# Kernel tuning notes

Hardware: AMD Instinct MI355X
Metric: run time of the kernel (lower is better)

Reference implementation:

```python
import jax, jax.numpy as jnp
import numpy as np

NUM_HEADS = 4
LN_EPS = 1e-5
L2_EPS = 1e-12


def setup_inputs() -> dict:
    key = jax.random.key(0)
    ks = jax.random.split(key, 10)
    B, L, D, Hd = 256, 197, 768, 512
    dh = Hd // NUM_HEADS  # 128
    NC = 1000
    sc = lambda k, shape, s: jax.random.normal(k, shape, jnp.float32) * s
    return {
        "cls_token": jax.random.normal(ks[0], (B, D), jnp.float32),
        "x": jax.random.normal(ks[1], (B, L, D), jnp.float32),
        "proj_w": sc(ks[2], (D, Hd), 0.02),
        "proj_b": jnp.zeros((Hd,), jnp.float32),
        "ln_g": jnp.ones((dh,), jnp.float32),
        "ln_b": jnp.zeros((dh,), jnp.float32),
        "conv1_w": sc(ks[3], (3, 3, 3, 3), 0.2),
        "conv2_w": sc(ks[4], (3, 3, 3, 3), 0.2),
        "cls1_w": sc(ks[5], (D, NC), 0.02),
        "cls1_b": jnp.zeros((NC,), jnp.float32),
        "cls2_w": sc(ks[6], (2883, NC), 0.02),
        "cls2_b": jnp.zeros((NC,), jnp.float32),
    }


def reference(cls_token, x, proj_w, proj_b, ln_g, ln_b, conv1_w, conv2_w,
              cls1_w, cls1_b, cls2_w, cls2_b):
    B, L, D = x.shape
    dh = ln_g.shape[0]
    # proj on patch tokens (drop cls at position 0)
    xp = x[:, 1:, :] @ proj_w + proj_b            # (B, 196, 512)
    Lp = xp.shape[1]
    H = xp.shape[2] // dh
    heads = xp.reshape(B, Lp, H, dh).transpose(2, 0, 1, 3)  # (H, B, Lp, dh)
    # LayerNorm over last dim (eps=1e-5, biased var, affine)
    mu = heads.mean(-1, keepdims=True)
    var = heads.var(-1, keepdims=True)
    hn = (heads - mu) * jax.lax.rsqrt(var + LN_EPS) * ln_g + ln_b
    # Covariance._remove_mean: adaptive_avg_pool2d on (B, dh, Lp) -> mean over BOTH dh and Lp per sample
    hn = hn - hn.mean(axis=(2, 3), keepdims=True)
    # 'near' cross-covariances between adjacent heads, all pairs batched
    x1, x2 = hn[:-1], hn[1:]                      # (H-1, B, Lp, dh)
    cov = jnp.einsum('pbnd,pbne->pbde', x1, x2) / Lp  # (H-1, B, dh, dh)
    # L2 normalize over dim=2 (row axis of each dh x dh map), F.normalize eps
    nrm = jnp.sqrt(jnp.sum(cov * cov, axis=2, keepdims=True))
    cov = cov / jnp.maximum(nrm, L2_EPS)
    cov = cov.transpose(1, 0, 2, 3)               # (B, 3, 128, 128)
    conv = lambda z, w: jax.lax.conv_general_dilated(
        z, w, (2, 2), 'VALID', dimension_numbers=('NCHW', 'OIHW', 'NCHW'))
    z = conv(cov, conv1_w)                        # (B, 3, 63, 63)
    z = jax.nn.gelu(z, approximate=False)
    z = conv(z, conv2_w)                          # (B, 3, 31, 31)
    flat = z.reshape(B, -1)                       # (B, 2883)
    out = ((cls_token @ cls1_w + cls1_b) + (flat @ cls2_w + cls2_b)) / 2
    return out
```

## Files before the change

### kernel.cpp

```cpp
#include <hip/hip_runtime.h>
#include <hip/hip_bf16.h>
#include <cstdint>

typedef __bf16 bf16_t;
typedef __bf16 bf16x4 __attribute__((ext_vector_type(4)));
typedef __bf16 bf16x8 __attribute__((ext_vector_type(8)));
typedef float floatx4 __attribute__((ext_vector_type(4)));

#define LNEPS 1e-5f

__device__ inline void async_copy16(const bf16_t* g, bf16_t* l) {
    __builtin_amdgcn_global_load_lds((const __attribute__((address_space(1))) void*)g,
                                     (__attribute__((address_space(3))) void*)l,
                                     16, 0, 0);
}

__global__ __launch_bounds__(256)
void k_cvt_x(const float* __restrict__ x, bf16_t* __restrict__ xbf) {
    const int vid = blockIdx.x * 256 + threadIdx.x;
    const int row = vid / 96;
    const int kv  = vid - row * 96;
    const int b = row / 196, l = row - (row / 196) * 196;
    const float* src = x + ((b * 197 + l + 1) * 96 + kv) * 8;
    const floatx4 f0 = *(const floatx4*)src;
    const floatx4 f1 = *(const floatx4*)(src + 4);
    bf16x8 o;
#pragma unroll
    for (int e = 0; e < 4; e++) { o[e] = (bf16_t)f0[e]; o[e+4] = (bf16_t)f1[e]; }
    *(bf16x8*)(xbf + vid * 8) = o;
}

__global__ __launch_bounds__(256)
void k_transpose_w(const float* __restrict__ w, bf16_t* __restrict__ wt) {
    __shared__ bf16_t tile[32][33];
    const int bx = blockIdx.x;
    const int by = blockIdx.y;
    const int tx = threadIdx.x & 31, ty = threadIdx.x >> 5;
    for (int i = ty; i < 32; i += 8)
        tile[i][tx] = (bf16_t)w[(by*32 + i)*512 + bx*32 + tx];
    __syncthreads();
    for (int i = ty; i < 32; i += 8)
        wt[(bx*32 + i)*768 + by*32 + tx] = tile[tx][i];
}

__global__ __launch_bounds__(256, 3)
void k_proj_ln(const bf16_t* __restrict__ xbf, const bf16_t* __restrict__ wt,
               const float* __restrict__ pb, const float* __restrict__ lng,
               const float* __restrict__ lnb, bf16_t* __restrict__ hn)
{
    __shared__ bf16_t As[2][128*32];
    __shared__ bf16_t Bs[2][128*32];

    const int t = threadIdx.x;
    const int lane = t & 63;
    const int wv = t >> 6;
    const int q = lane >> 4;
    const int c = lane & 15;
    const int h  = blockIdx.x;
    const int m0 = blockIdx.y * 128;

    const int srow  = t >> 2;
    const int skoff = (t & 3) * 8;
    const bf16_t* ag = xbf + (m0 + srow) * 768 + skoff;
    const bf16_t* bg = wt + (h*128 + srow) * 768 + skoff;

    floatx4 acc[2][8];
#pragma unroll
    for (int i = 0; i < 2; i++)
#pragma unroll
        for (int j = 0; j < 8; j++)
#pragma unroll
            for (int r = 0; r < 4; r++) acc[i][j][r] = 0.f;

    async_copy16(ag,           &As[0][t*8]);
    async_copy16(ag + 64*768,  &As[0][2048 + t*8]);
    async_copy16(bg,           &Bs[0][t*8]);
    async_copy16(bg + 64*768,  &Bs[0][2048 + t*8]);
    __syncthreads();

    int buf = 0;
    for (int ks = 0; ks < 24; ks++) {
        if (ks < 23) {
            const int kn = (ks + 1) * 32;
            async_copy16(ag + kn,           &As[buf^1][t*8]);
            async_copy16(ag + 64*768 + kn,  &As[buf^1][2048 + t*8]);
            async_copy16(bg + kn,           &Bs[buf^1][t*8]);
            async_copy16(bg + 64*768 + kn,  &Bs[buf^1][2048 + t*8]);
        }
        bf16x8 af[2], bfr[8];
#pragma unroll
        for (int i = 0; i < 2; i++)
            af[i] = *(const bf16x8*)&As[buf][(wv*32 + i*16 + c)*32 + q*8];
#pragma unroll
        for (int j = 0; j < 8; j++)
            bfr[j] = *(const bf16x8*)&Bs[buf][(j*16 + c)*32 + q*8];
#pragma unroll
        for (int i = 0; i < 2; i++)
#pragma unroll
            for (int j = 0; j < 8; j++)
                acc[i][j] = __builtin_amdgcn_mfma_f32_16x16x32_bf16(af[i], bfr[j], acc[i][j], 0, 0, 0);
        __syncthreads();
        buf ^= 1;
    }

    float bias[8], gg[8], bb[8];
#pragma unroll
    for (int j = 0; j < 8; j++) {
        const int d = j*16 + c;
        bias[j] = pb[h*128 + d];
        gg[j]   = lng[d];
        bb[j]   = lnb[d];
    }
#pragma unroll
    for (int i = 0; i < 2; i++) {
#pragma unroll
        for (int r = 0; r < 4; r++) {
            float s = 0.f, s2 = 0.f;
#pragma unroll
            for (int j = 0; j < 8; j++) {
                const float v = acc[i][j][r] + bias[j];
                acc[i][j][r] = v;
                s += v; s2 += v*v;
            }
#pragma unroll
            for (int o = 1; o < 16; o <<= 1) { s += __shfl_xor(s, o); s2 += __shfl_xor(s2, o); }
            const float mu = s * (1.f/128.f);
            const float ms = s2 * (1.f/128.f);
            const float rstd = rsqrtf(ms - mu*mu + LNEPS);
            const int gm = m0 + wv*32 + i*16 + q*4 + r;
            const int bI = gm / 196, l = gm - bI*196;
            bf16_t* dst = hn + (((h*256 + bI)*196 + l) << 7);
#pragma unroll
            for (int j = 0; j < 8; j++) {
                const float v = (acc[i][j][r] - mu)*rstd*gg[j] + bb[j];
                dst[j*16 + c] = (bf16_t)v;
            }
        }
    }
}

__global__ __launch_bounds__(256)
void k_colsum(const bf16_t* __restrict__ hn, float* __restrict__ colsum)
{
    __shared__ float tmp[16][128];
    const int t = threadIdx.x;
    const int g = t >> 4;
    const int dv = t & 15;
    const bf16_t* S = hn + ((long)blockIdx.x * 196 << 7) + dv * 8;
    float s[8] = {0.f,0.f,0.f,0.f,0.f,0.f,0.f,0.f};
    for (int n = g; n < 196; n += 16) {
        const bf16x8 v = *(const bf16x8*)(S + (n << 7));
#pragma unroll
        for (int e = 0; e < 8; e++) s[e] += (float)v[e];
    }
#pragma unroll
    for (int e = 0; e < 8; e++) tmp[g][dv*8 + e] = s[e];
    __syncthreads();
    if (t < 128) {
        float a = 0.f;
#pragma unroll
        for (int g2 = 0; g2 < 16; g2++) a += tmp[g2][t];
        colsum[(blockIdx.x << 7) + t] = a;
    }
}

__global__ __launch_bounds__(256, 2)
void k_cov(const bf16_t* __restrict__ hn, const float* __restrict__ colsum,
           float* __restrict__ cov)
{
    __shared__ bf16_t x1s[128*40];
    __shared__ bf16_t x2s[128*40];
    __shared__ float rs1[128], rs2[128];
    __shared__ float colsq[2][128];
    __shared__ float nrm_inv[128];
    __shared__ float mu_s[2];

    const int t = threadIdx.x;
    const int lane = t & 63;
    const int wv = t >> 6;
    const int wr = wv >> 1, wc = wv & 1;
    const int q = lane >> 4;
    const int c = lane & 15;
    const int b = blockIdx.x;
    const int p = blockIdx.y;

    const bf16_t* X1 = hn + (((p*256 + b)*196) << 7);
    const bf16_t* X2 = hn + ((((p+1)*256 + b)*196) << 7);

    if (t < 128) rs1[t] = colsum[((p*256 + b) << 7) + t];
    else         rs2[t & 127] = colsum[(((p+1)*256 + b) << 7) + (t & 127)];
    __syncthreads();
    if (wv == 0) {
        float s = rs1[lane] + rs1[lane + 64];
#pragma unroll
        for (int o = 1; o < 64; o <<= 1) s += __shfl_xor(s, o);
        if (lane == 0) mu_s[0] = s * (1.f/(196.f*128.f));
    } else if (wv == 1) {
        float s = rs2[lane] + rs2[lane + 64];
#pragma unroll
        for (int o = 1; o < 64; o <<= 1) s += __shfl_xor(s, o);
        if (lane == 0) mu_s[1] = s * (1.f/(196.f*128.f));
    }

    floatx4 acc[4][4];
#pragma unroll
    for (int i = 0; i < 4; i++)
#pragma unroll
        for (int j = 0; j < 4; j++)
#pragma unroll
            for (int r = 0; r < 4; r++) acc[i][j][r] = 0.f;

    const int nl = t >> 3;
    const int d0 = (t & 7) * 16;

    for (int n0 = 0; n0 < 224; n0 += 32) {
        __syncthreads();
        const int n = n0 + nl;
        bf16x8 va, vb, wa, wb;
        if (n < 196) {
            const bf16_t* s1 = X1 + (n << 7) + d0;
            const bf16_t* s2 = X2 + (n << 7) + d0;
            va = *(const bf16x8*)s1;
            vb = *(const bf16x8*)(s1 + 8);
            wa = *(const bf16x8*)s2;
            wb = *(const bf16x8*)(s2 + 8);
        } else {
#pragma unroll
            for (int e = 0; e < 8; e++) {
                va[e] = (bf16_t)0.f; vb[e] = (bf16_t)0.f;
                wa[e] = (bf16_t)0.f; wb[e] = (bf16_t)0.f;
            }
        }
#pragma unroll
        for (int e = 0; e < 8; e++) {
            x1s[(d0 + e)*40 + nl]     = va[e];
            x1s[(d0 + 8 + e)*40 + nl] = vb[e];
            x2s[(d0 + e)*40 + nl]     = wa[e];
            x2s[(d0 + 8 + e)*40 + nl] = wb[e];
        }
        __syncthreads();
        bf16x8 af[4], bfr[4];
#pragma unroll
        for (int i = 0; i < 4; i++)
            af[i] = *(const bf16x8*)&x1s[(wr*64 + i*16 + c)*40 + q*8];
#pragma unroll
        for (int j = 0; j < 4; j++)
            bfr[j] = *(const bf16x8*)&x2s[(wc*64 + j*16 + c)*40 + q*8];
#pragma unroll
        for (int i = 0; i < 4; i++)
#pragma unroll
            for (int j = 0; j < 4; j++)
                acc[i][j] = __builtin_amdgcn_mfma_f32_16x16x32_bf16(af[i], bfr[j], acc[i][j], 0, 0, 0);
    }

    const float mu1 = mu_s[0], mu2 = mu_s[1];
    const float invL = 1.f/196.f;
    float csq[4] = {0.f, 0.f, 0.f, 0.f};
#pragma unroll
    for (int i = 0; i < 4; i++)
#pragma unroll
        for (int j = 0; j < 4; j++)
#pragma unroll
            for (int r = 0; r < 4; r++) {
                const int d = wr*64 + i*16 + q*4 + r;
                const int e = wc*64 + j*16 + c;
                const float v = acc[i][j][r]*invL - mu2*rs1[d]*invL - mu1*rs2[e]*invL + mu1*mu2;
                acc[i][j][r] = v;
                csq[j] += v*v;
            }
#pragma unroll
    for (int j = 0; j < 4; j++) {
        float s = csq[j];
        s += __shfl_xor(s, 16);
        s += __shfl_xor(s, 32);
        csq[j] = s;
    }
    if (q == 0) {
#pragma unroll
        for (int j = 0; j < 4; j++) colsq[wr][wc*64 + j*16 + c] = csq[j];
    }
    __syncthreads();
    if (t < 128) {
        const float nr = sqrtf(colsq[0][t] + colsq[1][t]);
        nrm_inv[t] = 1.f / fmaxf(nr, 1e-12f);
    }
    __syncthreads();
    float* dst = cov + ((long)b*3 + p)*16384;
#pragma unroll
    for (int i = 0; i < 4; i++)
#pragma unroll
        for (int j = 0; j < 4; j++) {
            const int e = wc*64 + j*16 + c;
            const float ni = nrm_inv[e];
#pragma unroll
            for (int r = 0; r < 4; r++) {
                const int d = wr*64 + i*16 + q*4 + r;
                dst[(d << 7) + e] = acc[i][j][r] * ni;
            }
        }
}

__global__ __launch_bounds__(256)
void k_convs(const float* __restrict__ cov, const float* __restrict__ w1,
             const float* __restrict__ w2, bf16_t* __restrict__ Xb)
{
    __shared__ float Z[3*3969];
    __shared__ float W1s[81];
    __shared__ float W2s[81];
    const int t = threadIdx.x, b = blockIdx.x;
    if (t < 81) { W1s[t] = w1[t]; W2s[t] = w2[t]; }
    __syncthreads();
    const float* C = cov + (long)b*3*16384;
    for (int idx = t; idx < 3*3969; idx += 256) {
        const int o = idx / 3969, rem = idx - o*3969;
        const int y = rem / 63, xx = rem - y*63;
        float a = 0.f;
#pragma unroll
        for (int i = 0; i < 3; i++) {
            const float* Ci = C + i*16384 + (2*y)*128 + 2*xx;
            const float* Wi = &W1s[o*27 + i*9];
            a += Ci[0]*Wi[0]   + Ci[1]*Wi[1]   + Ci[2]*Wi[2]
               + Ci[128]*Wi[3] + Ci[129]*Wi[4] + Ci[130]*Wi[5]
               + Ci[256]*Wi[6] + Ci[257]*Wi[7] + Ci[258]*Wi[8];
        }
        Z[idx] = 0.5f*a*(1.0f + erff(a*0.70710678118654752f));
    }
    __syncthreads();
    for (int idx = t; idx < 2883; idx += 256) {
        const int o = idx / 961, rem = idx - o*961;
        const int y = rem / 31, xx = rem - y*31;
        float a = 0.f;
#pragma unroll
        for (int i = 0; i < 3; i++) {
            const float* Zi = Z + i*3969 + (2*y)*63 + 2*xx;
            const float* Wi = &W2s[(o*3+i)*9];
            a += Zi[0]*Wi[0]   + Zi[1]*Wi[1]   + Zi[2]*Wi[2]
               + Zi[63]*Wi[3]  + Zi[64]*Wi[4]  + Zi[65]*Wi[5]
               + Zi[126]*Wi[6] + Zi[127]*Wi[7] + Zi[128]*Wi[8];
        }
        Xb[(long)b*3712 + 768 + idx] = (bf16_t)a;
    }
}

__global__ __launch_bounds__(256)
void k_cvt_cls(const float* __restrict__ cls, bf16_t* __restrict__ Xb)
{
    const int t = threadIdx.x, b = blockIdx.x;
    for (int k = t; k < 768; k += 256)
        Xb[b*3712 + k] = (bf16_t)cls[b*768 + k];
    if (t < 61) Xb[b*3712 + 3651 + t] = (bf16_t)0.f;
}

__global__ __launch_bounds__(256)
void k_cvt_w(const float* __restrict__ W1, const float* __restrict__ W2,
             bf16_t* __restrict__ Wb)
{
    __shared__ bf16_t tile[32][33];
    const int k0 = blockIdx.x * 32;
    const int n0 = blockIdx.y * 32;
    const int tx = threadIdx.x & 31, ty = threadIdx.x >> 5;
    for (int i = ty; i < 32; i += 8) {
        const int k = k0 + i, n = n0 + tx;
        float v = 0.f;
        if (n < 1000 && k < 3651)
            v = (k < 768) ? W1[k*1000 + n] : W2[(k-768)*1000 + n];
        tile[i][tx] = (bf16_t)v;
    }
    __syncthreads();
    for (int i = ty; i < 32; i += 8)
        Wb[(n0 + i)*3712 + k0 + tx] = tile[tx][i];
}

__global__ __launch_bounds__(256, 2)
void k_gemm_cls(const bf16_t* __restrict__ Xb, const bf16_t* __restrict__ Wb,
                float* __restrict__ partial)
{
    __shared__ bf16_t As[128*32];
    __shared__ bf16_t Bs[128*32];

    const int t = threadIdx.x;
    const int lane = t & 63;
    const int wv = t >> 6;
    const int wr = wv >> 1, wc = wv & 1;
    const int q = lane >> 4;
    const int c = lane & 15;
    const int nt = blockIdx.x;
    const int mt = blockIdx.y;
    const int sp = blockIdx.z;

    const int srow  = t >> 2;
    const int skoff = (t & 3) * 8;
    const int m0 = mt * 128, n0 = nt * 128;
    const int kbase = sp * 928;
    const bf16_t* ag0 = Xb + (m0 + srow) * 3712 + kbase + skoff;
    const bf16_t* ag1 = Xb + (m0 + srow + 64) * 3712 + kbase + skoff;
    const bf16_t* bg0 = Wb + (n0 + srow) * 3712 + kbase + skoff;
    const bf16_t* bg1 = Wb + (n0 + srow + 64) * 3712 + kbase + skoff;

    floatx4 acc[4][4];
#pragma unroll
    for (int i = 0; i < 4; i++)
#pragma unroll
        for (int j = 0; j < 4; j++)
#pragma unroll
            for (int r = 0; r < 4; r++) acc[i][j][r] = 0.f;

    for (int k0 = 0; k0 < 928; k0 += 32) {
        __syncthreads();
        async_copy16(ag0 + k0, &As[t*8]);
        async_copy16(ag1 + k0, &As[2048 + t*8]);
        async_copy16(bg0 + k0, &Bs[t*8]);
        async_copy16(bg1 + k0, &Bs[2048 + t*8]);
        __syncthreads();
        bf16x8 af[4], bfr[4];
#pragma unroll
        for (int i = 0; i < 4; i++)
            af[i] = *(const bf16x8*)&As[(wr*64 + i*16 + c)*32 + q*8];
#pragma unroll
        for (int j = 0; j < 4; j++)
            bfr[j] = *(const bf16x8*)&Bs[(wc*64 + j*16 + c)*32 + q*8];
#pragma unroll
        for (int i = 0; i < 4; i++)
#pragma unroll
            for (int j = 0; j < 4; j++)
                acc[i][j] = __builtin_amdgcn_mfma_f32_16x16x32_bf16(af[i], bfr[j], acc[i][j], 0, 0, 0);
    }

    float* base = partial + ((long)sp*256 + m0)*1024 + n0;
#pragma unroll
    for (int i = 0; i < 4; i++)
#pragma unroll
        for (int r = 0; r < 4; r++) {
            const int row = wr*64 + i*16 + q*4 + r;
#pragma unroll
            for (int j = 0; j < 4; j++)
                base[row*1024 + wc*64 + j*16 + c] = acc[i][j][r];
        }
}

__global__ __launch_bounds__(256)
void k_cls_fin(const float* __restrict__ partial, const float* __restrict__ b1,
               const float* __restrict__ b2, float* __restrict__ out)
{
    const int idx = blockIdx.x * 256 + threadIdx.x;
    const int m = idx / 1000, n = idx - m*1000;
    float s = partial[(m)*1024 + n] + partial[(256 + m)*1024 + n]
            + partial[(512 + m)*1024 + n] + partial[(768 + m)*1024 + n];
    out[idx] = 0.5f*(s + b1[n] + b2[n]);
}

extern "C" void kernel_launch(void* const* d_in, const int* in_sizes, int n_in,
                              void* d_out, int out_size, void* d_ws, size_t ws_size,
                              hipStream_t stream) {
    const float* cls = (const float*)d_in[0];
    const float* x   = (const float*)d_in[1];
    const float* pw  = (const float*)d_in[2];
    const float* pb  = (const float*)d_in[3];
    const float* lng = (const float*)d_in[4];
    const float* lnb = (const float*)d_in[5];
    const float* c1w = (const float*)d_in[6];
    const float* c2w = (const float*)d_in[7];
    const float* w1  = (const float*)d_in[8];
    const float* b1  = (const float*)d_in[9];
    const float* w2  = (const float*)d_in[10];
    const float* b2  = (const float*)d_in[11];

    char* ws = (char*)d_ws;
    bf16_t* hn    = (bf16_t*)(ws);
    bf16_t* xbf   = (bf16_t*)(ws + 51380224ull);
    bf16_t* wt    = (bf16_t*)(ws + 128450560ull);
    float*  covb  = (float*) (ws + 51380224ull);
    float*  csum  = (float*) (ws + 129236992ull);
    bf16_t* Xb    = (bf16_t*)(ws + 129761280ull);
    bf16_t* Wb    = (bf16_t*)(ws + 131661824ull);
    float*  part  = (float*) (ws + 139264000ull);
    float*  out   = (float*)d_out;

    k_transpose_w<<<dim3(16, 24), 256, 0, stream>>>(pw, wt);
    k_cvt_x<<<18816, 256, 0, stream>>>(x, xbf);
    k_cvt_cls<<<256, 256, 0, stream>>>(cls, Xb);
    k_cvt_w<<<dim3(116, 32), 256, 0, stream>>>(w1, w2, Wb);
    k_proj_ln<<<dim3(4, 392), 256, 0, stream>>>(xbf, wt, pb, lng, lnb, hn);
    k_colsum<<<1024, 256, 0, stream>>>(hn, csum);
    k_cov<<<dim3(256, 3), 256, 0, stream>>>(hn, csum, covb);
    k_convs<<<256, 256, 0, stream>>>(covb, c1w, c2w, Xb);
    k_gemm_cls<<<dim3(8, 2, 4), 256, 0, stream>>>(Xb, Wb, part);
    k_cls_fin<<<1000, 256, 0, stream>>>(part, b1, b2, out);
}
```

Measured before the change: 439.4 us.

## Fuse fp32-to-bf16 conversion and column sums into projection kernel; split convs

The projection+LayerNorm kernel now reads fp32 activations directly, converts them to bf16 in registers and stores them to LDS, so the separate conversion pass and its bf16 intermediate buffer go away. The per-sample column sums are accumulated in the epilogue and added with atomics, which removes the separate colsum kernel (the sums are zeroed in the cls conversion kernel). The conv kernel is split into two row halves per sample to double the block count. The A loads are now synchronous register loads instead of async LDS copies, which may expose latency, and the fp32 atomics make the summation order nondeterministic.

```diff
diff --git a/kernel.cpp b/kernel.cpp
--- a/kernel.cpp
+++ b/kernel.cpp
@@ -13,21 +13,6 @@
     __builtin_amdgcn_global_load_lds((const __attribute__((address_space(1))) void*)g,
                                      (__attribute__((address_space(3))) void*)l,
                                      16, 0, 0);
-}
-
-__global__ __launch_bounds__(256)
-void k_cvt_x(const float* __restrict__ x, bf16_t* __restrict__ xbf) {
-    const int vid = blockIdx.x * 256 + threadIdx.x;
-    const int row = vid / 96;
-    const int kv  = vid - row * 96;
-    const int b = row / 196, l = row - (row / 196) * 196;
-    const float* src = x + ((b * 197 + l + 1) * 96 + kv) * 8;
-    const floatx4 f0 = *(const floatx4*)src;
-    const floatx4 f1 = *(const floatx4*)(src + 4);
-    bf16x8 o;
-#pragma unroll
-    for (int e = 0; e < 4; e++) { o[e] = (bf16_t)f0[e]; o[e+4] = (bf16_t)f1[e]; }
-    *(bf16x8*)(xbf + vid * 8) = o;
 }
 
 __global__ __launch_bounds__(256)
@@ -44,9 +29,10 @@
 }
 
 __global__ __launch_bounds__(256, 3)
-void k_proj_ln(const bf16_t* __restrict__ xbf, const bf16_t* __restrict__ wt,
+void k_proj_ln(const float* __restrict__ x, const bf16_t* __restrict__ wt,
                const float* __restrict__ pb, const float* __restrict__ lng,
-               const float* __restrict__ lnb, bf16_t* __restrict__ hn)
+               const float* __restrict__ lnb, bf16_t* __restrict__ hn,
+               float* __restrict__ csum)
 {
     __shared__ bf16_t As[2][128*32];
     __shared__ bf16_t Bs[2][128*32];
@@ -59,9 +45,15 @@
     const int h  = blockIdx.x;
     const int m0 = blockIdx.y * 128;
 
+    const int arow = t >> 1;
+    const int acol = (t & 1) * 16;
+    const int agm  = m0 + arow;
+    const int ab   = agm / 196;
+    const int al   = agm - ab * 196;
+    const float* ag = x + ((long)(ab * 197 + al + 1) * 768) + acol;
+
     const int srow  = t >> 2;
     const int skoff = (t & 3) * 8;
-    const bf16_t* ag = xbf + (m0 + srow) * 768 + skoff;
     const bf16_t* bg = wt + (h*128 + srow) * 768 + skoff;
 
     floatx4 acc[2][8];
@@ -72,20 +64,35 @@
 #pragma unroll
             for (int r = 0; r < 4; r++) acc[i][j][r] = 0.f;
 
-    async_copy16(ag,           &As[0][t*8]);
-    async_copy16(ag + 64*768,  &As[0][2048 + t*8]);
-    async_copy16(bg,           &Bs[0][t*8]);
-    async_copy16(bg + 64*768,  &Bs[0][2048 + t*8]);
+    floatx4 a0 = *(const floatx4*)(ag);
+    floatx4 a1 = *(const floatx4*)(ag + 4);
+    floatx4 a2 = *(const floatx4*)(ag + 8);
+    floatx4 a3 = *(const floatx4*)(ag + 12);
+    async_copy16(bg,          &Bs[0][t*8]);
+    async_copy16(bg + 64*768, &Bs[0][2048 + t*8]);
+    {
+        bf16x8 w0, w1;
+#pragma unroll
+        for (int e = 0; e < 4; e++) {
+            w0[e] = (bf16_t)a0[e]; w0[e+4] = (bf16_t)a1[e];
+            w1[e] = (bf16_t)a2[e]; w1[e+4] = (bf16_t)a3[e];
+        }
+        *(bf16x8*)&As[0][arow*32 + acol]     = w0;
+        *(bf16x8*)&As[0][arow*32 + acol + 8] = w1;
+    }
     __syncthreads();
 
     int buf = 0;
     for (int ks = 0; ks < 24; ks++) {
+        const int nbuf = buf ^ 1;
         if (ks < 23) {
             const int kn = (ks + 1) * 32;
-            async_copy16(ag + kn,           &As[buf^1][t*8]);
-            async_copy16(ag + 64*768 + kn,  &As[buf^1][2048 + t*8]);
-            async_copy16(bg + kn,           &Bs[buf^1][t*8]);
-            async_copy16(bg + 64*768 + kn,  &Bs[buf^1][2048 + t*8]);
+            a0 = *(const floatx4*)(ag + kn);
+            a1 = *(const floatx4*)(ag + kn + 4);
+            a2 = *(const floatx4*)(ag + kn + 8);
+            a3 = *(const floatx4*)(ag + kn + 12);
+            async_copy16(bg + kn,          &Bs[nbuf][t*8]);
+            async_copy16(bg + 64*768 + kn, &Bs[nbuf][2048 + t*8]);
         }
         bf16x8 af[2], bfr[8];
 #pragma unroll
@@ -99,8 +106,18 @@
 #pragma unroll
             for (int j = 0; j < 8; j++)
                 acc[i][j] = __builtin_amdgcn_mfma_f32_16x16x32_bf16(af[i], bfr[j], acc[i][j], 0, 0, 0);
+        if (ks < 23) {
+            bf16x8 w0, w1;
+#pragma unroll
+            for (int e = 0; e < 4; e++) {
+                w0[e] = (bf16_t)a0[e]; w0[e+4] = (bf16_t)a1[e];
+                w1[e] = (bf16_t)a2[e]; w1[e+4] = (bf16_t)a3[e];
+            }
+            *(bf16x8*)&As[nbuf][arow*32 + acol]     = w0;
+            *(bf16x8*)&As[nbuf][arow*32 + acol + 8] = w1;
+        }
         __syncthreads();
-        buf ^= 1;
+        buf = nbuf;
     }
 
     float bias[8], gg[8], bb[8];
@@ -111,6 +128,11 @@
         gg[j]   = lng[d];
         bb[j]   = lnb[d];
     }
+    float cs0[8], cs1[8];
+#pragma unroll
+    for (int j = 0; j < 8; j++) { cs0[j] = 0.f; cs1[j] = 0.f; }
+    const int b0 = m0 / 196;
+    const int bL = (m0 + 127) / 196;
 #pragma unroll
     for (int i = 0; i < 2; i++) {
 #pragma unroll
@@ -130,37 +152,35 @@
             const int gm = m0 + wv*32 + i*16 + q*4 + r;
             const int bI = gm / 196, l = gm - bI*196;
             bf16_t* dst = hn + (((h*256 + bI)*196 + l) << 7);
+            const bool first = (bI == b0);
 #pragma unroll
             for (int j = 0; j < 8; j++) {
                 const float v = (acc[i][j][r] - mu)*rstd*gg[j] + bb[j];
                 dst[j*16 + c] = (bf16_t)v;
+                cs0[j] += first ? v : 0.f;
+                cs1[j] += first ? 0.f : v;
             }
         }
     }
-}
-
-__global__ __launch_bounds__(256)
-void k_colsum(const bf16_t* __restrict__ hn, float* __restrict__ colsum)
-{
-    __shared__ float tmp[16][128];
-    const int t = threadIdx.x;
-    const int g = t >> 4;
-    const int dv = t & 15;
-    const bf16_t* S = hn + ((long)blockIdx.x * 196 << 7) + dv * 8;
-    float s[8] = {0.f,0.f,0.f,0.f,0.f,0.f,0.f,0.f};
-    for (int n = g; n < 196; n += 16) {
-        const bf16x8 v = *(const bf16x8*)(S + (n << 7));
-#pragma unroll
-        for (int e = 0; e < 8; e++) s[e] += (float)v[e];
-    }
-#pragma unroll
-    for (int e = 0; e < 8; e++) tmp[g][dv*8 + e] = s[e];
-    __syncthreads();
-    if (t < 128) {
-        float a = 0.f;
-#pragma unroll
-        for (int g2 = 0; g2 < 16; g2++) a += tmp[g2][t];
-        colsum[(blockIdx.x << 7) + t] = a;
+    float* scr = (float*)As;
+#pragma unroll
+    for (int j = 0; j < 8; j++) {
+        float s0 = cs0[j], s1 = cs1[j];
+        s0 += __shfl_xor(s0, 16); s0 += __shfl_xor(s0, 32);
+        s1 += __shfl_xor(s1, 16); s1 += __shfl_xor(s1, 32);
+        if (q == 0) {
+            scr[(wv*2 + 0)*128 + j*16 + c] = s0;
+            scr[(wv*2 + 1)*128 + j*16 + c] = s1;
+        }
+    }
+    __syncthreads();
+    {
+        const int bucket = t >> 7, d = t & 127;
+        if (bucket == 0 || bL > b0) {
+            const float s = scr[(0*2 + bucket)*128 + d] + scr[(1*2 + bucket)*128 + d]
+                          + scr[(2*2 + bucket)*128 + d] + scr[(3*2 + bucket)*128 + d];
+            atomicAdd(&csum[((h*256 + b0 + bucket) << 7) + d], s);
+        }
     }
 }
 
@@ -304,16 +324,23 @@
 void k_convs(const float* __restrict__ cov, const float* __restrict__ w1,
              const float* __restrict__ w2, bf16_t* __restrict__ Xb)
 {
-    __shared__ float Z[3*3969];
+    __shared__ float Z[3*33*63];
     __shared__ float W1s[81];
     __shared__ float W2s[81];
-    const int t = threadIdx.x, b = blockIdx.x;
+    const int t = threadIdx.x;
+    const int b = blockIdx.x >> 1, half = blockIdx.x & 1;
+    const int zy0 = half ? 32 : 0;
+    const int nzy = half ? 31 : 33;
+    const int y20 = half ? 16 : 0;
+    const int ny2 = half ? 15 : 16;
     if (t < 81) { W1s[t] = w1[t]; W2s[t] = w2[t]; }
     __syncthreads();
     const float* C = cov + (long)b*3*16384;
-    for (int idx = t; idx < 3*3969; idx += 256) {
-        const int o = idx / 3969, rem = idx - o*3969;
-        const int y = rem / 63, xx = rem - y*63;
+    const int ztot = 3*nzy*63;
+    for (int idx = t; idx < ztot; idx += 256) {
+        const int o = idx / (nzy*63), rem = idx - o*(nzy*63);
+        const int yl = rem / 63, xx = rem - yl*63;
+        const int y = zy0 + yl;
         float a = 0.f;
 #pragma unroll
         for (int i = 0; i < 3; i++) {
@@ -323,32 +350,37 @@
                + Ci[128]*Wi[3] + Ci[129]*Wi[4] + Ci[130]*Wi[5]
                + Ci[256]*Wi[6] + Ci[257]*Wi[7] + Ci[258]*Wi[8];
         }
-        Z[idx] = 0.5f*a*(1.0f + erff(a*0.70710678118654752f));
-    }
-    __syncthreads();
-    for (int idx = t; idx < 2883; idx += 256) {
-        const int o = idx / 961, rem = idx - o*961;
-        const int y = rem / 31, xx = rem - y*31;
+        Z[o*2079 + yl*63 + xx] = 0.5f*a*(1.0f + erff(a*0.70710678118654752f));
+    }
+    __syncthreads();
+    const int c2tot = 3*ny2*31;
+    for (int idx = t; idx < c2tot; idx += 256) {
+        const int o = idx / (ny2*31), rem = idx - o*(ny2*31);
+        const int y2l = rem / 31, x2 = rem - y2l*31;
         float a = 0.f;
 #pragma unroll
         for (int i = 0; i < 3; i++) {
-            const float* Zi = Z + i*3969 + (2*y)*63 + 2*xx;
+            const float* Zi = Z + i*2079 + (2*y2l)*63 + 2*x2;
             const float* Wi = &W2s[(o*3+i)*9];
             a += Zi[0]*Wi[0]   + Zi[1]*Wi[1]   + Zi[2]*Wi[2]
                + Zi[63]*Wi[3]  + Zi[64]*Wi[4]  + Zi[65]*Wi[5]
                + Zi[126]*Wi[6] + Zi[127]*Wi[7] + Zi[128]*Wi[8];
         }
-        Xb[(long)b*3712 + 768 + idx] = (bf16_t)a;
+        const int oy2 = y20 + y2l;
+        Xb[(long)b*3712 + 768 + o*961 + oy2*31 + x2] = (bf16_t)a;
     }
 }
 
 __global__ __launch_bounds__(256)
-void k_cvt_cls(const float* __restrict__ cls, bf16_t* __restrict__ Xb)
+void k_cvt_cls(const float* __restrict__ cls, bf16_t* __restrict__ Xb,
+               float* __restrict__ csum)
 {
     const int t = threadIdx.x, b = blockIdx.x;
     for (int k = t; k < 768; k += 256)
         Xb[b*3712 + k] = (bf16_t)cls[b*768 + k];
     if (t < 61) Xb[b*3712 + 3651 + t] = (bf16_t)0.f;
+    float* cz = csum + b*512;
+    cz[t] = 0.f; cz[t + 256] = 0.f;
 }
 
 __global__ __launch_bounds__(256)
@@ -467,9 +499,8 @@
 
     char* ws = (char*)d_ws;
     bf16_t* hn    = (bf16_t*)(ws);
-    bf16_t* xbf   = (bf16_t*)(ws + 51380224ull);
+    float*  covb  = (float*) (ws + 51380224ull);
     bf16_t* wt    = (bf16_t*)(ws + 128450560ull);
-    float*  covb  = (float*) (ws + 51380224ull);
     float*  csum  = (float*) (ws + 129236992ull);
     bf16_t* Xb    = (bf16_t*)(ws + 129761280ull);
     bf16_t* Wb    = (bf16_t*)(ws + 131661824ull);
@@ -477,13 +508,11 @@
     float*  out   = (float*)d_out;
 
     k_transpose_w<<<dim3(16, 24), 256, 0, stream>>>(pw, wt);
-    k_cvt_x<<<18816, 256, 0, stream>>>(x, xbf);
-    k_cvt_cls<<<256, 256, 0, stream>>>(cls, Xb);
+    k_cvt_cls<<<256, 256, 0, stream>>>(cls, Xb, csum);
     k_cvt_w<<<dim3(116, 32), 256, 0, stream>>>(w1, w2, Wb);
-    k_proj_ln<<<dim3(4, 392), 256, 0, stream>>>(xbf, wt, pb, lng, lnb, hn);
-    k_colsum<<<1024, 256, 0, stream>>>(hn, csum);
+    k_proj_ln<<<dim3(4, 392), 256, 0, stream>>>(x, wt, pb, lng, lnb, hn, csum);
     k_cov<<<dim3(256, 3), 256, 0, stream>>>(hn, csum, covb);
-    k_convs<<<256, 256, 0, stream>>>(covb, c1w, c2w, Xb);
+    k_convs<<<512, 256, 0, stream>>>(covb, c1w, c2w, Xb);
     k_gemm_cls<<<dim3(8, 2, 4), 256, 0, stream>>>(Xb, Wb, part);
     k_cls_fin<<<1000, 256, 0, stream>>>(part, b1, b2, out);
 }
```

Measured after the change: 455.7 us. 3.7% more time.
